# Kernel optimization log

Measured on AMD Instinct MI355X. Metric: run time of the kernel, lower is better.

Reference implementation:

```python
import jax, jax.numpy as jnp
import numpy as np

LN_EPS = 1e-5  # torch nn.LayerNorm default


def setup_inputs() -> dict:
    key = jax.random.key(0)
    kx, kw = jax.random.split(key)
    tokens, d_in, d_out = 8192, 4096, 16384
    x = jax.random.normal(kx, (tokens, d_in), dtype=jnp.float32)
    # nn.Linear weight layout: [out_features, in_features]
    W = jax.random.normal(kw, (d_out, d_in), dtype=jnp.float32) * (1.0 / np.sqrt(d_in))
    return {"x": x, "W": W}


def reference(x, W):
    # LayerNorm over last dim, no affine params (elementwise_affine=False)
    mean = jnp.mean(x, axis=-1, keepdims=True)
    var = jnp.mean(jnp.square(x - mean), axis=-1, keepdims=True)  # biased, as torch LN
    xn = (x - mean) * jax.lax.rsqrt(var + LN_EPS)
    # Linear (no bias): [tokens, d_in] @ [d_in, d_out]
    y = jnp.einsum("td,od->to", xn, W)
    return jax.nn.sigmoid(y)
```

## Files before the change

kernel.cpp:

```cpp
#include <hip/hip_runtime.h>
#include <hip/hip_bf16.h>
#include <stdint.h>

#define TOKENS 8192
#define DIN    4096
#define DOUT   16384

#define BM 256
#define BN 256
#define BKT 64
#define NT (DIN / BKT)
#define NJ (NT / 2)

typedef short s16x8 __attribute__((ext_vector_type(8)));
typedef float f32x4 __attribute__((ext_vector_type(4)));

#define AS1 __attribute__((address_space(1)))
#define AS3 __attribute__((address_space(3)))
#define VMCNT(n)  asm volatile("s_waitcnt vmcnt(" #n ")" ::: "memory")
#define SCHEDB()  __builtin_amdgcn_sched_barrier(0)
#define BAR()     __builtin_amdgcn_s_barrier()

__device__ __forceinline__ unsigned short f2bf(float f) {
  unsigned int u = __float_as_uint(f);
  u += 0x7fffu + ((u >> 16) & 1u);
  return (unsigned short)(u >> 16);
}

__global__ __launch_bounds__(256) void ln_kernel(const float* __restrict__ x,
                                                 unsigned short* __restrict__ xn) {
  const int row = blockIdx.x;
  const float4* xr = reinterpret_cast<const float4*>(x + (size_t)row * DIN);
  float4 v[4];
  float sum = 0.f, ssq = 0.f;
#pragma unroll
  for (int i = 0; i < 4; ++i) {
    v[i] = xr[threadIdx.x + i * 256];
    sum += v[i].x + v[i].y + v[i].z + v[i].w;
    ssq += v[i].x * v[i].x + v[i].y * v[i].y + v[i].z * v[i].z + v[i].w * v[i].w;
  }
#pragma unroll
  for (int off = 32; off > 0; off >>= 1) {
    sum += __shfl_xor(sum, off, 64);
    ssq += __shfl_xor(ssq, off, 64);
  }
  __shared__ float red[8];
  const int wid = threadIdx.x >> 6;
  if ((threadIdx.x & 63) == 0) { red[wid] = sum; red[wid + 4] = ssq; }
  __syncthreads();
  sum = red[0] + red[1] + red[2] + red[3];
  ssq = red[4] + red[5] + red[6] + red[7];
  const float mean = sum * (1.f / DIN);
  const float var  = ssq * (1.f / DIN) - mean * mean;
  const float rs   = rsqrtf(var + 1e-5f);
  ushort4* xo = reinterpret_cast<ushort4*>(xn + (size_t)row * DIN);
#pragma unroll
  for (int i = 0; i < 4; ++i) {
    ushort4 o;
    o.x = f2bf((v[i].x - mean) * rs);
    o.y = f2bf((v[i].y - mean) * rs);
    o.z = f2bf((v[i].z - mean) * rs);
    o.w = f2bf((v[i].w - mean) * rs);
    xo[threadIdx.x + i * 256] = o;
  }
}

__global__ __launch_bounds__(256) void cvt_kernel(const float* __restrict__ W,
                                                  unsigned short* __restrict__ Wb) {
  const size_t i = (size_t)blockIdx.x * 256 + threadIdx.x;
  float4 v = reinterpret_cast<const float4*>(W)[i];
  ushort4 o;
  o.x = f2bf(v.x); o.y = f2bf(v.y); o.z = f2bf(v.z); o.w = f2bf(v.w);
  reinterpret_cast<ushort4*>(Wb)[i] = o;
}

__global__ __launch_bounds__(512, 2) void gemm_sig(const unsigned short* __restrict__ A,
                                                   const unsigned short* __restrict__ B,
                                                   float* __restrict__ C) {
  __shared__ unsigned short Asl[2 * 256 * 64];
  __shared__ unsigned short Bsl[2 * 256 * 64];

  const int bid = blockIdx.x;
  const int cpx = gridDim.x >> 3;
  const int swz = (bid & 7) * cpx + (bid >> 3);
  const int bm = swz & 31;
  const int bn = swz >> 5;

  const int tid  = threadIdx.x;
  const int wid  = tid >> 6;
  const int lane = tid & 63;
  const int wr = wid >> 2, wc = wid & 3;

  const unsigned short* gA = A + (size_t)bm * BM * DIN;
  const unsigned short* gB = B + (size_t)bn * BN * DIN;

  const int l8 = lane >> 3, l7 = lane & 7;
  const int csw = l7 ^ l8;
  const unsigned short* sA = gA + (size_t)(wid * 8 + l8) * DIN + csw * 8;
  const unsigned short* sB = gB + (size_t)(wid * 8 + l8) * DIN + csw * 8;
  const int dOfs = wid * 512;

#define STG_Aq(p, q, kt) __builtin_amdgcn_global_load_lds( \
    (const AS1 void*)(sA + (size_t)(q) * 64 * DIN + (size_t)(kt) * BKT), \
    (AS3 void*)(Asl + ((p) * 256 + (q) * 64) * 64 + dOfs), 16, 0, 0)
#define STG_Bq(p, q, kt) __builtin_amdgcn_global_load_lds( \
    (const AS1 void*)(sB + (size_t)(q) * 64 * DIN + (size_t)(kt) * BKT), \
    (AS3 void*)(Bsl + ((p) * 256 + (q) * 64) * 64 + dOfs), 16, 0, 0)

  int aO[8], bO[4], slt[2];
#pragma unroll
  for (int m = 0; m < 8; ++m) aO[m] = (wr * 128 + m * 16 + (lane & 15)) * 64;
#pragma unroll
  for (int n = 0; n < 4; ++n) bO[n] = (wc * 64 + n * 16 + (lane & 15)) * 64;
  slt[0] = ((lane >> 4) ^ l7) * 8;
  slt[1] = (((lane >> 4) + 4) ^ l7) * 8;

  s16x8 af[4], bf0[4], bf1[4];
  f32x4 acc[8][4] = {};

#define RD_A(p, mb4, kh) do { _Pragma("unroll") for (int mm = 0; mm < 4; ++mm) \
    af[mm] = *reinterpret_cast<const s16x8*>(Asl + (p) * 16384 + aO[(mb4) + mm] + slt[kh]); } while (0)
#define RD_B(p, kh, dst) do { _Pragma("unroll") for (int nn = 0; nn < 4; ++nn) \
    dst[nn] = *reinterpret_cast<const s16x8*>(Bsl + (p) * 16384 + bO[nn] + slt[kh]); } while (0)
#define MM(mb4, bfr) do { _Pragma("unroll") for (int mm = 0; mm < 4; ++mm) \
    _Pragma("unroll") for (int nn = 0; nn < 4; ++nn) \
      acc[(mb4) + mm][nn] = __builtin_amdgcn_mfma_f32_16x16x32_bf16(af[mm], bfr[nn], acc[(mb4) + mm][nn], 0, 0, 0); } while (0)
#define PRIO1() __builtin_amdgcn_s_setprio(1)
#define PRIO0() __builtin_amdgcn_s_setprio(0)

  STG_Aq(0, 0, 0); STG_Aq(0, 1, 0); STG_Aq(0, 2, 0); STG_Aq(0, 3, 0);
  STG_Bq(0, 0, 0); STG_Bq(0, 1, 0); STG_Bq(0, 2, 0); STG_Bq(0, 3, 0);
  STG_Aq(1, 0, 1); STG_Aq(1, 2, 1);
  STG_Bq(1, 0, 1); STG_Bq(1, 1, 1); STG_Bq(1, 2, 1); STG_Bq(1, 3, 1);
  VMCNT(6); SCHEDB(); BAR();

  for (int j = 0; j < NJ - 1; ++j) {
    const int t1 = 2 * j + 1, t2 = 2 * j + 2, t3 = 2 * j + 3;
    VMCNT(8); RD_A(0, 0, 0); RD_B(0, 0, bf0);
    STG_Aq(1, 1, t1); STG_Aq(1, 3, t1);
    SCHEDB(); BAR(); PRIO1(); MM(0, bf0); PRIO0(); SCHEDB(); BAR();
    VMCNT(8); RD_A(0, 0, 1); RD_B(0, 1, bf1);
    SCHEDB(); BAR(); PRIO1(); MM(0, bf1); PRIO0(); SCHEDB(); BAR();
    VMCNT(8); RD_A(0, 4, 0);
    STG_Bq(0, 0, t2); STG_Bq(0, 1, t2); STG_Bq(0, 2, t2); STG_Bq(0, 3, t2);
    STG_Aq(0, 0, t2); STG_Aq(0, 2, t2);
    SCHEDB(); BAR(); PRIO1(); MM(4, bf0); PRIO0(); SCHEDB(); BAR();
    VMCNT(8); RD_A(0, 4, 1);
    SCHEDB(); BAR(); PRIO1(); MM(4, bf1); PRIO0(); SCHEDB(); BAR();
    VMCNT(8); RD_A(1, 0, 0); RD_B(1, 0, bf0);
    STG_Aq(0, 1, t2); STG_Aq(0, 3, t2);
    SCHEDB(); BAR(); PRIO1(); MM(0, bf0); PRIO0(); SCHEDB(); BAR();
    VMCNT(8); RD_A(1, 0, 1); RD_B(1, 1, bf1);
    SCHEDB(); BAR(); PRIO1(); MM(0, bf1); PRIO0(); SCHEDB(); BAR();
    VMCNT(8); RD_A(1, 4, 0);
    STG_Bq(1, 0, t3); STG_Bq(1, 1, t3); STG_Bq(1, 2, t3); STG_Bq(1, 3, t3);
    STG_Aq(1, 0, t3); STG_Aq(1, 2, t3);
    SCHEDB(); BAR(); PRIO1(); MM(4, bf0); PRIO0(); SCHEDB(); BAR();
    VMCNT(8); RD_A(1, 4, 1);
    SCHEDB(); BAR(); PRIO1(); MM(4, bf1); PRIO0(); SCHEDB(); BAR();
  }

  {
    const int t1 = NT - 1;
    VMCNT(8); RD_A(0, 0, 0); RD_B(0, 0, bf0);
    STG_Aq(1, 1, t1); STG_Aq(1, 3, t1);
    SCHEDB(); BAR(); PRIO1(); MM(0, bf0); PRIO0(); SCHEDB(); BAR();
    VMCNT(8); RD_A(0, 0, 1); RD_B(0, 1, bf1);
    SCHEDB(); BAR(); PRIO1(); MM(0, bf1); PRIO0(); SCHEDB(); BAR();
    VMCNT(8); RD_A(0, 4, 0);
    SCHEDB(); BAR(); PRIO1(); MM(4, bf0); PRIO0(); SCHEDB(); BAR();
    VMCNT(2); RD_A(0, 4, 1);
    SCHEDB(); BAR(); PRIO1(); MM(4, bf1); PRIO0(); SCHEDB(); BAR();
    VMCNT(2); RD_A(1, 0, 0); RD_B(1, 0, bf0);
    SCHEDB(); BAR(); PRIO1(); MM(0, bf0); PRIO0(); SCHEDB(); BAR();
    VMCNT(0); RD_A(1, 0, 1); RD_B(1, 1, bf1);
    SCHEDB(); BAR(); PRIO1(); MM(0, bf1); PRIO0(); SCHEDB(); BAR();
    VMCNT(0); RD_A(1, 4, 0);
    SCHEDB(); BAR(); PRIO1(); MM(4, bf0); PRIO0(); SCHEDB(); BAR();
    VMCNT(0); RD_A(1, 4, 1);
    SCHEDB(); BAR(); PRIO1(); MM(4, bf1); PRIO0();
  }

#undef STG_Aq
#undef STG_Bq
#undef RD_A
#undef RD_B
#undef MM

  const int crow0 = bm * BM + wr * 128 + (lane >> 4) * 4;
  const int ccol0 = bn * BN + wc * 64 + (lane & 15);
#pragma unroll
  for (int m = 0; m < 8; ++m)
#pragma unroll
    for (int n = 0; n < 4; ++n)
#pragma unroll
      for (int jj = 0; jj < 4; ++jj) {
        const float v = acc[m][n][jj];
        C[(size_t)(crow0 + m * 16 + jj) * DOUT + (ccol0 + n * 16)] = 1.f / (1.f + __expf(-v));
      }
}

extern "C" void kernel_launch(void* const* d_in, const int* in_sizes, int n_in,
                              void* d_out, int out_size, void* d_ws, size_t ws_size,
                              hipStream_t stream) {
  const float* x = (const float*)d_in[0];
  const float* W = (const float*)d_in[1];
  float* out = (float*)d_out;

  unsigned short* xn = (unsigned short*)d_ws;
  unsigned short* Wb = xn + (size_t)TOKENS * DIN;

  ln_kernel<<<TOKENS, 256, 0, stream>>>(x, xn);
  cvt_kernel<<<((size_t)DOUT * DIN) / 1024, 256, 0, stream>>>(W, Wb);
  gemm_sig<<<(TOKENS / BM) * (DOUT / BN), 512, 0, stream>>>(xn, Wb, out);
}
```

Before: 1.351 ms.

## Restructure GEMM main loop to read both k-halves per fragment and reschedule loads

The GEMM inner loop now loads both 32-wide k halves of each A/B fragment together and runs MFMA phases over 4x2 sub-tiles covering the full 64-wide k slice. Each phase issues fewer duplicate LDS reads of A. Global-to-LDS staging is redistributed across the phases, with explicit lgkmcnt waits and fewer vmcnt waits. The intent is to cut redundant LDS traffic and barrier stalls, at the cost of more live fragment registers and a riskier hand-tuned wait schedule that could race or stall.

Result: no change. 1.372 ms (+1.6%).

```diff
diff --git a/kernel.cpp b/kernel.cpp
--- a/kernel.cpp
+++ b/kernel.cpp
@@ -18,8 +18,12 @@
 #define AS1 __attribute__((address_space(1)))
 #define AS3 __attribute__((address_space(3)))
 #define VMCNT(n)  asm volatile("s_waitcnt vmcnt(" #n ")" ::: "memory")
+#define LGKM0()   asm volatile("s_waitcnt lgkmcnt(0)" ::: "memory")
+#define LGKM8()   asm volatile("s_waitcnt lgkmcnt(8)" ::: "memory")
 #define SCHEDB()  __builtin_amdgcn_sched_barrier(0)
 #define BAR()     __builtin_amdgcn_s_barrier()
+#define PRIO1()   __builtin_amdgcn_s_setprio(1)
+#define PRIO0()   __builtin_amdgcn_s_setprio(0)
 
 __device__ __forceinline__ unsigned short f2bf(float f) {
   unsigned int u = __float_as_uint(f);
@@ -107,85 +111,105 @@
     (const AS1 void*)(sB + (size_t)(q) * 64 * DIN + (size_t)(kt) * BKT), \
     (AS3 void*)(Bsl + ((p) * 256 + (q) * 64) * 64 + dOfs), 16, 0, 0)
 
-  int aO[8], bO[4], slt[2];
+  int aO[8], bO[4];
 #pragma unroll
   for (int m = 0; m < 8; ++m) aO[m] = (wr * 128 + m * 16 + (lane & 15)) * 64;
 #pragma unroll
   for (int n = 0; n < 4; ++n) bO[n] = (wc * 64 + n * 16 + (lane & 15)) * 64;
-  slt[0] = ((lane >> 4) ^ l7) * 8;
-  slt[1] = (((lane >> 4) + 4) ^ l7) * 8;
-
-  s16x8 af[4], bf0[4], bf1[4];
+  const int slt0 = ((lane >> 4) ^ l7) * 8;
+  const int slt1 = (((lane >> 4) + 4) ^ l7) * 8;
+
+  s16x8 a0[4], a1[4], b0k0[2], b0k1[2], b1k0[2], b1k1[2];
   f32x4 acc[8][4] = {};
 
-#define RD_A(p, mb4, kh) do { _Pragma("unroll") for (int mm = 0; mm < 4; ++mm) \
-    af[mm] = *reinterpret_cast<const s16x8*>(Asl + (p) * 16384 + aO[(mb4) + mm] + slt[kh]); } while (0)
-#define RD_B(p, kh, dst) do { _Pragma("unroll") for (int nn = 0; nn < 4; ++nn) \
-    dst[nn] = *reinterpret_cast<const s16x8*>(Bsl + (p) * 16384 + bO[nn] + slt[kh]); } while (0)
-#define MM(mb4, bfr) do { _Pragma("unroll") for (int mm = 0; mm < 4; ++mm) \
-    _Pragma("unroll") for (int nn = 0; nn < 4; ++nn) \
-      acc[(mb4) + mm][nn] = __builtin_amdgcn_mfma_f32_16x16x32_bf16(af[mm], bfr[nn], acc[(mb4) + mm][nn], 0, 0, 0); } while (0)
-#define PRIO1() __builtin_amdgcn_s_setprio(1)
-#define PRIO0() __builtin_amdgcn_s_setprio(0)
+#define RD_A2(p, mb4) do { _Pragma("unroll") for (int mm = 0; mm < 4; ++mm) { \
+    const unsigned short* _b = Asl + (p) * 16384 + aO[(mb4) + mm]; \
+    a0[mm] = *reinterpret_cast<const s16x8*>(_b + slt0); \
+    a1[mm] = *reinterpret_cast<const s16x8*>(_b + slt1); } } while (0)
+#define RD_B2(p, nb2, d0, d1) do { _Pragma("unroll") for (int nn = 0; nn < 2; ++nn) { \
+    const unsigned short* _b = Bsl + (p) * 16384 + bO[(nb2) + nn]; \
+    d0[nn] = *reinterpret_cast<const s16x8*>(_b + slt0); \
+    d1[nn] = *reinterpret_cast<const s16x8*>(_b + slt1); } } while (0)
+#define MM8(mb4, nb2, bk0, bk1) do { _Pragma("unroll") for (int mm = 0; mm < 4; ++mm) \
+    _Pragma("unroll") for (int nn = 0; nn < 2; ++nn) { \
+      acc[(mb4) + mm][(nb2) + nn] = __builtin_amdgcn_mfma_f32_16x16x32_bf16(a0[mm], bk0[nn], acc[(mb4) + mm][(nb2) + nn], 0, 0, 0); \
+      acc[(mb4) + mm][(nb2) + nn] = __builtin_amdgcn_mfma_f32_16x16x32_bf16(a1[mm], bk1[nn], acc[(mb4) + mm][(nb2) + nn], 0, 0, 0); } } while (0)
 
   STG_Aq(0, 0, 0); STG_Aq(0, 1, 0); STG_Aq(0, 2, 0); STG_Aq(0, 3, 0);
   STG_Bq(0, 0, 0); STG_Bq(0, 1, 0); STG_Bq(0, 2, 0); STG_Bq(0, 3, 0);
   STG_Aq(1, 0, 1); STG_Aq(1, 2, 1);
   STG_Bq(1, 0, 1); STG_Bq(1, 1, 1); STG_Bq(1, 2, 1); STG_Bq(1, 3, 1);
-  VMCNT(6); SCHEDB(); BAR();
+  STG_Aq(1, 1, 1); STG_Aq(1, 3, 1);
+  VMCNT(8); BAR();
 
   for (int j = 0; j < NJ - 1; ++j) {
-    const int t1 = 2 * j + 1, t2 = 2 * j + 2, t3 = 2 * j + 3;
-    VMCNT(8); RD_A(0, 0, 0); RD_B(0, 0, bf0);
-    STG_Aq(1, 1, t1); STG_Aq(1, 3, t1);
-    SCHEDB(); BAR(); PRIO1(); MM(0, bf0); PRIO0(); SCHEDB(); BAR();
-    VMCNT(8); RD_A(0, 0, 1); RD_B(0, 1, bf1);
-    SCHEDB(); BAR(); PRIO1(); MM(0, bf1); PRIO0(); SCHEDB(); BAR();
-    VMCNT(8); RD_A(0, 4, 0);
-    STG_Bq(0, 0, t2); STG_Bq(0, 1, t2); STG_Bq(0, 2, t2); STG_Bq(0, 3, t2);
+    const int t2 = 2 * j + 2, t3 = 2 * j + 3;
+    RD_A2(0, 0); RD_B2(0, 0, b0k0, b0k1);
+    LGKM8();
+    BAR(); LGKM0(); SCHEDB();
+    PRIO1(); MM8(0, 0, b0k0, b0k1); PRIO0(); BAR();
+    RD_B2(0, 2, b1k0, b1k1);
     STG_Aq(0, 0, t2); STG_Aq(0, 2, t2);
-    SCHEDB(); BAR(); PRIO1(); MM(4, bf0); PRIO0(); SCHEDB(); BAR();
-    VMCNT(8); RD_A(0, 4, 1);
-    SCHEDB(); BAR(); PRIO1(); MM(4, bf1); PRIO0(); SCHEDB(); BAR();
-    VMCNT(8); RD_A(1, 0, 0); RD_B(1, 0, bf0);
-    STG_Aq(0, 1, t2); STG_Aq(0, 3, t2);
-    SCHEDB(); BAR(); PRIO1(); MM(0, bf0); PRIO0(); SCHEDB(); BAR();
-    VMCNT(8); RD_A(1, 0, 1); RD_B(1, 1, bf1);
-    SCHEDB(); BAR(); PRIO1(); MM(0, bf1); PRIO0(); SCHEDB(); BAR();
-    VMCNT(8); RD_A(1, 4, 0);
-    STG_Bq(1, 0, t3); STG_Bq(1, 1, t3); STG_Bq(1, 2, t3); STG_Bq(1, 3, t3);
+    BAR(); LGKM0(); SCHEDB();
+    PRIO1(); MM8(0, 2, b1k0, b1k1); PRIO0(); BAR();
+    RD_A2(0, 4);
+    STG_Bq(0, 0, t2); STG_Bq(0, 1, t2);
+    BAR(); LGKM0(); SCHEDB();
+    PRIO1(); MM8(4, 0, b0k0, b0k1); PRIO0(); BAR();
+    VMCNT(4);
+    STG_Bq(0, 2, t2); STG_Bq(0, 3, t2); STG_Aq(0, 1, t2); STG_Aq(0, 3, t2);
+    BAR();
+    PRIO1(); MM8(4, 2, b1k0, b1k1); PRIO0(); BAR();
+    RD_A2(1, 0); RD_B2(1, 0, b0k0, b0k1);
+    LGKM8();
+    BAR(); LGKM0(); SCHEDB();
+    PRIO1(); MM8(0, 0, b0k0, b0k1); PRIO0(); BAR();
+    RD_B2(1, 2, b1k0, b1k1);
     STG_Aq(1, 0, t3); STG_Aq(1, 2, t3);
-    SCHEDB(); BAR(); PRIO1(); MM(4, bf0); PRIO0(); SCHEDB(); BAR();
-    VMCNT(8); RD_A(1, 4, 1);
-    SCHEDB(); BAR(); PRIO1(); MM(4, bf1); PRIO0(); SCHEDB(); BAR();
+    BAR(); LGKM0(); SCHEDB();
+    PRIO1(); MM8(0, 2, b1k0, b1k1); PRIO0(); BAR();
+    RD_A2(1, 4);
+    STG_Bq(1, 0, t3); STG_Bq(1, 1, t3);
+    BAR(); LGKM0(); SCHEDB();
+    PRIO1(); MM8(4, 0, b0k0, b0k1); PRIO0(); BAR();
+    VMCNT(4);
+    STG_Bq(1, 2, t3); STG_Bq(1, 3, t3); STG_Aq(1, 1, t3); STG_Aq(1, 3, t3);
+    BAR();
+    PRIO1(); MM8(4, 2, b1k0, b1k1); PRIO0(); BAR();
   }
 
   {
-    const int t1 = NT - 1;
-    VMCNT(8); RD_A(0, 0, 0); RD_B(0, 0, bf0);
-    STG_Aq(1, 1, t1); STG_Aq(1, 3, t1);
-    SCHEDB(); BAR(); PRIO1(); MM(0, bf0); PRIO0(); SCHEDB(); BAR();
-    VMCNT(8); RD_A(0, 0, 1); RD_B(0, 1, bf1);
-    SCHEDB(); BAR(); PRIO1(); MM(0, bf1); PRIO0(); SCHEDB(); BAR();
-    VMCNT(8); RD_A(0, 4, 0);
-    SCHEDB(); BAR(); PRIO1(); MM(4, bf0); PRIO0(); SCHEDB(); BAR();
-    VMCNT(2); RD_A(0, 4, 1);
-    SCHEDB(); BAR(); PRIO1(); MM(4, bf1); PRIO0(); SCHEDB(); BAR();
-    VMCNT(2); RD_A(1, 0, 0); RD_B(1, 0, bf0);
-    SCHEDB(); BAR(); PRIO1(); MM(0, bf0); PRIO0(); SCHEDB(); BAR();
-    VMCNT(0); RD_A(1, 0, 1); RD_B(1, 1, bf1);
-    SCHEDB(); BAR(); PRIO1(); MM(0, bf1); PRIO0(); SCHEDB(); BAR();
-    VMCNT(0); RD_A(1, 4, 0);
-    SCHEDB(); BAR(); PRIO1(); MM(4, bf0); PRIO0(); SCHEDB(); BAR();
-    VMCNT(0); RD_A(1, 4, 1);
-    SCHEDB(); BAR(); PRIO1(); MM(4, bf1); PRIO0();
+    RD_A2(0, 0); RD_B2(0, 0, b0k0, b0k1);
+    LGKM8();
+    BAR(); LGKM0(); SCHEDB();
+    PRIO1(); MM8(0, 0, b0k0, b0k1); PRIO0(); BAR();
+    RD_B2(0, 2, b1k0, b1k1);
+    BAR(); LGKM0(); SCHEDB();
+    PRIO1(); MM8(0, 2, b1k0, b1k1); PRIO0(); BAR();
+    RD_A2(0, 4);
+    BAR(); LGKM0(); SCHEDB();
+    PRIO1(); MM8(4, 0, b0k0, b0k1); PRIO0(); BAR();
+    VMCNT(0);
+    BAR();
+    PRIO1(); MM8(4, 2, b1k0, b1k1); PRIO0(); BAR();
+    RD_A2(1, 0); RD_B2(1, 0, b0k0, b0k1);
+    LGKM8();
+    BAR(); LGKM0(); SCHEDB();
+    PRIO1(); MM8(0, 0, b0k0, b0k1); PRIO0(); BAR();
+    RD_B2(1, 2, b1k0, b1k1);
+    BAR(); LGKM0(); SCHEDB();
+    PRIO1(); MM8(0, 2, b1k0, b1k1); PRIO0(); BAR();
+    RD_A2(1, 4);
+    BAR(); LGKM0(); SCHEDB();
+    PRIO1(); MM8(4, 0, b0k0, b0k1); PRIO0(); BAR();
+    PRIO1(); MM8(4, 2, b1k0, b1k1); PRIO0();
   }
 
 #undef STG_Aq
 #undef STG_Bq
-#undef RD_A
-#undef RD_B
-#undef MM
+#undef RD_A2
+#undef RD_B2
+#undef MM8
 
   const int crow0 = bm * BM + wr * 128 + (lane >> 4) * 4;
   const int ccol0 = bn * BN + wc * 64 + (lane & 15);
```
